# Kernel optimization log

Hardware: AMD Instinct MI355X
Metric: run time of the kernel (lower is better)

The kernel has to match this reference:

```python
import jax, jax.numpy as jnp
import numpy as np

BS, S, H, T = 16, 256, 1024, 32  # batch, num entities, hidden, num relation tags
N_TAGS = 7


def setup_inputs() -> dict:
    key = jax.random.key(0)
    k0, k1, k2, k3 = jax.random.split(key, 4)
    seq_embedding = jax.random.normal(k0, (BS, H), dtype=jnp.float32)
    entities_embeddings = jax.random.normal(k1, (BS, S, H), dtype=jnp.float32)
    entities_tags = jax.random.randint(k2, (BS, S), 0, N_TAGS)
    # relation_classifier: Linear(3*H -> T)
    W = jax.random.normal(k3, (T, 3 * H), dtype=jnp.float32) * 0.02
    b = jnp.zeros((T,), dtype=jnp.float32)
    return {
        "seq_embedding": seq_embedding,
        "entities_embeddings": entities_embeddings,
        "W": W,
        "b": b,
        "entities_tags": entities_tags,
    }


def reference(seq_embedding, entities_embeddings, W, b, entities_tags):
    # Original (eval mode, dropout=identity):
    #   pred[b,i,j] = W @ concat(E[b,i], E[b,j], S[b]) + bias
    # (arg1/arg2/all_seq linears and tag embeddings are dead code in the
    #  original forward: their outputs are never used.)
    # Decompose W = [W1 | W2 | W3] along the feature axis; mathematically
    # identical to materializing the (bs,S,S,3H) concat tensor.
    h = entities_embeddings.shape[-1]
    W1, W2, W3 = W[:, :h], W[:, h:2 * h], W[:, 2 * h:]
    p1 = jnp.einsum('bih,th->bit', entities_embeddings, W1)  # arg1 contribution
    p2 = jnp.einsum('bjh,th->bjt', entities_embeddings, W2)  # arg2 contribution
    ps = seq_embedding @ W3.T + b                             # seq + bias
    # (bs, S, S, T)
    return p1[:, :, None, :] + p2[:, None, :, :] + ps[:, None, None, :]
```

## Files before the change

kernel.cpp:

```cpp
#include <hip/hip_runtime.h>

#define BS 16
#define S  256
#define H  1024
#define T  32

#define PS_OFF 0
#define P1_OFF 512
#define P2_OFF (P1_OFF + BS * S * T)

typedef __bf16 bf16x8 __attribute__((ext_vector_type(8)));
typedef float  f32x4  __attribute__((ext_vector_type(4)));

__global__ __launch_bounds__(256) void gemm_ps(
    const float* __restrict__ seq, const float* __restrict__ E,
    const float* __restrict__ W, const float* __restrict__ bias,
    float* __restrict__ ws)
{
    const int tid = threadIdx.x;
    const int lane = tid & 63, wv = tid >> 6;

    if (blockIdx.x >= 256) {
        float* ps = ws + PS_OFF;
        const int o = (blockIdx.x - 256) * 4 + wv;
        const int bb = o >> 5, t = o & 31;
        const float4* sp = (const float4*)(seq + (size_t)bb * H) + lane * 4;
        const float4* wp = (const float4*)(W + (size_t)t * (3 * H) + 2 * H) + lane * 4;
        float acc = 0.f;
        #pragma unroll
        for (int k = 0; k < 4; ++k) {
            float4 a = sp[k], w = wp[k];
            acc += a.x * w.x + a.y * w.y + a.z * w.z + a.w * w.w;
        }
        #pragma unroll
        for (int m = 32; m >= 1; m >>= 1) acc += __shfl_xor(acc, m);
        if (lane == 0) ps[o] = acc + bias[t];
        return;
    }

    const int m0 = blockIdx.x * 16;
    const int nb = wv * 16;
    const int wrow = nb + (lane & 15);
    const int ksub = (lane >> 4) * 8;

    const float* wbase = W + (size_t)(wrow & 31) * (3 * H) + ((wrow >> 5) ? H : 0) + ksub;
    const float* ebase = E + (size_t)(m0 + (lane & 15)) * H + ksub;

    f32x4 acc[4] = {{0.f,0.f,0.f,0.f},{0.f,0.f,0.f,0.f},
                    {0.f,0.f,0.f,0.f},{0.f,0.f,0.f,0.f}};

    #pragma unroll 8
    for (int s = 0; s < 32; ++s) {
        float4 al = *(const float4*)(ebase + s * 32);
        float4 ah = *(const float4*)(ebase + s * 32 + 4);
        float4 bl = *(const float4*)(wbase + s * 32);
        float4 bh = *(const float4*)(wbase + s * 32 + 4);
        bf16x8 a, b;
        a[0] = (__bf16)al.x; a[1] = (__bf16)al.y; a[2] = (__bf16)al.z; a[3] = (__bf16)al.w;
        a[4] = (__bf16)ah.x; a[5] = (__bf16)ah.y; a[6] = (__bf16)ah.z; a[7] = (__bf16)ah.w;
        b[0] = (__bf16)bl.x; b[1] = (__bf16)bl.y; b[2] = (__bf16)bl.z; b[3] = (__bf16)bl.w;
        b[4] = (__bf16)bh.x; b[5] = (__bf16)bh.y; b[6] = (__bf16)bh.z; b[7] = (__bf16)bh.w;
        acc[s & 3] = __builtin_amdgcn_mfma_f32_16x16x32_bf16(a, b, acc[s & 3], 0, 0, 0);
    }
    f32x4 sum = (acc[0] + acc[1]) + (acc[2] + acc[3]);

    const int orow = (lane >> 4) * 4;
    float* dst = (nb < 32) ? (ws + P1_OFF) : (ws + P2_OFF);
    const int c = wrow & 31;
    #pragma unroll
    for (int r = 0; r < 4; ++r)
        dst[(size_t)(m0 + orow + r) * T + c] = sum[r];
}

__global__ __launch_bounds__(256) void bcast_add(
    const float* __restrict__ ws, float* __restrict__ out)
{
    const int blk = blockIdx.x;
    const int b = blk >> 8, i = blk & 255;
    const int tid = threadIdx.x;

    __shared__ __align__(16) float s1[32];
    if (tid < 32)
        s1[tid] = (ws + P1_OFF)[(size_t)(b * S + i) * T + tid]
                + (ws + PS_OFF)[b * T + tid];
    __syncthreads();

    const float4 s = *(const float4*)&s1[(tid & 7) * 4];
    const float4* p2v = (const float4*)(ws + P2_OFF) + (size_t)b * (S * T / 4);
    float4* ov = (float4*)out + (size_t)(b * S + i) * (S * T / 4);

    #pragma unroll
    for (int k = tid; k < S * T / 4; k += 256) {
        float4 v = p2v[k];
        float4 r;
        r.x = v.x + s.x; r.y = v.y + s.y; r.z = v.z + s.z; r.w = v.w + s.w;
        ov[k] = r;
    }
}

extern "C" void kernel_launch(void* const* d_in, const int* in_sizes, int n_in,
                              void* d_out, int out_size, void* d_ws, size_t ws_size,
                              hipStream_t stream)
{
    const float* seq  = (const float*)d_in[0];
    const float* E    = (const float*)d_in[1];
    const float* W    = (const float*)d_in[2];
    const float* bias = (const float*)d_in[3];
    float* out = (float*)d_out;
    float* ws  = (float*)d_ws;

    gemm_ps<<<384, 256, 0, stream>>>(seq, E, W, bias, ws);
    bcast_add<<<BS * S, 256, 0, stream>>>(ws, out);
}
```

Measured before the change: 45.25 us.

## Stage E tile in LDS for GEMM and emit four rows per broadcast block

The GEMM blocks now load their 16-row E tile cooperatively into shared memory in two K-halves, and prefetch the W fragments into registers, instead of each wave reading E directly from global memory. The seq-projection blocks move to the front of the grid. The broadcast-add kernel now handles four i-rows per block, so each P2 vector read is reused for four output rows and the grid shrinks by four. The broadcast-add stage writes the large output tensor and is bandwidth-bound, so the effect depends mostly on that store path. The GEMM change adds barriers and LDS use.

```diff
diff --git a/kernel.cpp b/kernel.cpp
--- a/kernel.cpp
+++ b/kernel.cpp
@@ -12,6 +12,13 @@
 typedef __bf16 bf16x8 __attribute__((ext_vector_type(8)));
 typedef float  f32x4  __attribute__((ext_vector_type(4)));
 
+__device__ inline bf16x8 to_bf8(float4 lo, float4 hi) {
+    bf16x8 r;
+    r[0] = (__bf16)lo.x; r[1] = (__bf16)lo.y; r[2] = (__bf16)lo.z; r[3] = (__bf16)lo.w;
+    r[4] = (__bf16)hi.x; r[5] = (__bf16)hi.y; r[6] = (__bf16)hi.z; r[7] = (__bf16)hi.w;
+    return r;
+}
+
 __global__ __launch_bounds__(256) void gemm_ps(
     const float* __restrict__ seq, const float* __restrict__ E,
     const float* __restrict__ W, const float* __restrict__ bias,
@@ -20,9 +27,9 @@
     const int tid = threadIdx.x;
     const int lane = tid & 63, wv = tid >> 6;
 
-    if (blockIdx.x >= 256) {
+    if (blockIdx.x < 128) {
         float* ps = ws + PS_OFF;
-        const int o = (blockIdx.x - 256) * 4 + wv;
+        const int o = blockIdx.x * 4 + wv;
         const int bb = o >> 5, t = o & 31;
         const float4* sp = (const float4*)(seq + (size_t)bb * H) + lane * 4;
         const float4* wp = (const float4*)(W + (size_t)t * (3 * H) + 2 * H) + lane * 4;
@@ -38,30 +45,70 @@
         return;
     }
 
-    const int m0 = blockIdx.x * 16;
+    __shared__ __align__(16) float Ef[16][516];
+
+    const int m0 = (blockIdx.x - 128) * 16;
     const int nb = wv * 16;
     const int wrow = nb + (lane & 15);
     const int ksub = (lane >> 4) * 8;
+    const int erow = lane & 15;
 
-    const float* wbase = W + (size_t)(wrow & 31) * (3 * H) + ((wrow >> 5) ? H : 0) + ksub;
-    const float* ebase = E + (size_t)(m0 + (lane & 15)) * H + ksub;
+    const float* wbase = W + (size_t)(wrow & 31) * (3 * H)
+                           + ((wrow >> 5) ? H : 0) + ksub;
 
     f32x4 acc[4] = {{0.f,0.f,0.f,0.f},{0.f,0.f,0.f,0.f},
                     {0.f,0.f,0.f,0.f},{0.f,0.f,0.f,0.f}};
 
-    #pragma unroll 8
-    for (int s = 0; s < 32; ++s) {
-        float4 al = *(const float4*)(ebase + s * 32);
-        float4 ah = *(const float4*)(ebase + s * 32 + 4);
-        float4 bl = *(const float4*)(wbase + s * 32);
-        float4 bh = *(const float4*)(wbase + s * 32 + 4);
-        bf16x8 a, b;
-        a[0] = (__bf16)al.x; a[1] = (__bf16)al.y; a[2] = (__bf16)al.z; a[3] = (__bf16)al.w;
-        a[4] = (__bf16)ah.x; a[5] = (__bf16)ah.y; a[6] = (__bf16)ah.z; a[7] = (__bf16)ah.w;
-        b[0] = (__bf16)bl.x; b[1] = (__bf16)bl.y; b[2] = (__bf16)bl.z; b[3] = (__bf16)bl.w;
-        b[4] = (__bf16)bh.x; b[5] = (__bf16)bh.y; b[6] = (__bf16)bh.z; b[7] = (__bf16)bh.w;
-        acc[s & 3] = __builtin_amdgcn_mfma_f32_16x16x32_bf16(a, b, acc[s & 3], 0, 0, 0);
+    float4 tmp[8];
+    #pragma unroll
+    for (int i = 0; i < 8; ++i) {
+        int f = tid + i * 256, row = f >> 7, c4 = f & 127;
+        tmp[i] = *(const float4*)(E + (size_t)(m0 + row) * H + c4 * 4);
     }
+    #pragma unroll
+    for (int i = 0; i < 8; ++i) {
+        int f = tid + i * 256, row = f >> 7, c4 = f & 127;
+        *(float4*)&Ef[row][c4 * 4] = tmp[i];
+    }
+    bf16x8 bf[16];
+    #pragma unroll
+    for (int s = 0; s < 16; ++s)
+        bf[s] = to_bf8(*(const float4*)(wbase + s * 32),
+                       *(const float4*)(wbase + s * 32 + 4));
+    __syncthreads();
+
+    #pragma unroll
+    for (int s = 0; s < 16; ++s) {
+        const float* e = &Ef[erow][s * 32 + ksub];
+        bf16x8 a = to_bf8(*(const float4*)e, *(const float4*)(e + 4));
+        acc[s & 3] = __builtin_amdgcn_mfma_f32_16x16x32_bf16(a, bf[s], acc[s & 3], 0, 0, 0);
+    }
+
+    #pragma unroll
+    for (int i = 0; i < 8; ++i) {
+        int f = tid + i * 256, row = f >> 7, c4 = f & 127;
+        tmp[i] = *(const float4*)(E + (size_t)(m0 + row) * H + 512 + c4 * 4);
+    }
+    #pragma unroll
+    for (int s = 0; s < 16; ++s)
+        bf[s] = to_bf8(*(const float4*)(wbase + 512 + s * 32),
+                       *(const float4*)(wbase + 512 + s * 32 + 4));
+
+    __syncthreads();
+    #pragma unroll
+    for (int i = 0; i < 8; ++i) {
+        int f = tid + i * 256, row = f >> 7, c4 = f & 127;
+        *(float4*)&Ef[row][c4 * 4] = tmp[i];
+    }
+    __syncthreads();
+
+    #pragma unroll
+    for (int s = 0; s < 16; ++s) {
+        const float* e = &Ef[erow][s * 32 + ksub];
+        bf16x8 a = to_bf8(*(const float4*)e, *(const float4*)(e + 4));
+        acc[s & 3] = __builtin_amdgcn_mfma_f32_16x16x32_bf16(a, bf[s], acc[s & 3], 0, 0, 0);
+    }
+
     f32x4 sum = (acc[0] + acc[1]) + (acc[2] + acc[3]);
 
     const int orow = (lane >> 4) * 4;
@@ -76,25 +123,40 @@
     const float* __restrict__ ws, float* __restrict__ out)
 {
     const int blk = blockIdx.x;
-    const int b = blk >> 8, i = blk & 255;
+    const int b  = blk >> 6;
+    const int i0 = (blk & 63) * 4;
     const int tid = threadIdx.x;
 
-    __shared__ __align__(16) float s1[32];
-    if (tid < 32)
-        s1[tid] = (ws + P1_OFF)[(size_t)(b * S + i) * T + tid]
-                + (ws + PS_OFF)[b * T + tid];
+    __shared__ __align__(16) float s1[4][32];
+    if (tid < 128) {
+        int r = tid >> 5, t = tid & 31;
+        s1[r][t] = (ws + P1_OFF)[(size_t)(b * S + i0 + r) * T + t]
+                 + (ws + PS_OFF)[b * T + t];
+    }
     __syncthreads();
 
-    const float4 s = *(const float4*)&s1[(tid & 7) * 4];
+    const int t4 = (tid & 7) * 4;
+    const float4 s0 = *(const float4*)&s1[0][t4];
+    const float4 s1v = *(const float4*)&s1[1][t4];
+    const float4 s2 = *(const float4*)&s1[2][t4];
+    const float4 s3 = *(const float4*)&s1[3][t4];
+
     const float4* p2v = (const float4*)(ws + P2_OFF) + (size_t)b * (S * T / 4);
-    float4* ov = (float4*)out + (size_t)(b * S + i) * (S * T / 4);
+    float4* o0 = (float4*)out + (size_t)(b * S + i0) * (S * T / 4);
+    const int RS = S * T / 4;
 
     #pragma unroll
-    for (int k = tid; k < S * T / 4; k += 256) {
+    for (int k = tid; k < RS; k += 256) {
         float4 v = p2v[k];
-        float4 r;
-        r.x = v.x + s.x; r.y = v.y + s.y; r.z = v.z + s.z; r.w = v.w + s.w;
-        ov[k] = r;
+        float4 r0, r1, r2, r3;
+        r0.x = v.x + s0.x;  r0.y = v.y + s0.y;  r0.z = v.z + s0.z;  r0.w = v.w + s0.w;
+        r1.x = v.x + s1v.x; r1.y = v.y + s1v.y; r1.z = v.z + s1v.z; r1.w = v.w + s1v.w;
+        r2.x = v.x + s2.x;  r2.y = v.y + s2.y;  r2.z = v.z + s2.z;  r2.w = v.w + s2.w;
+        r3.x = v.x + s3.x;  r3.y = v.y + s3.y;  r3.z = v.z + s3.z;  r3.w = v.w + s3.w;
+        o0[k]          = r0;
+        o0[k + RS]     = r1;
+        o0[k + 2 * RS] = r2;
+        o0[k + 3 * RS] = r3;
     }
 }
 
@@ -110,5 +172,5 @@
     float* ws  = (float*)d_ws;
 
     gemm_ps<<<384, 256, 0, stream>>>(seq, E, W, bias, ws);
-    bcast_add<<<BS * S, 256, 0, stream>>>(ws, out);
+    bcast_add<<<1024, 256, 0, stream>>>(ws, out);
 }
```

After: 53.26 us. 1.18x slower.

## Stage E tile in LDS as bf16 and split K across waves

Applied to the files above, without the earlier changes.

The GEMM part of gemm_ps now loads each 16-row E tile once into shared memory as bf16, instead of having each of the four waves read the same E rows from global memory. Each wave handles a quarter of K for all 64 output columns, holding its W fragments in registers. Partial sums are then reduced across waves through shared memory. The ps blocks are moved to the front of the grid. This cuts redundant global E traffic and conversion work, at the cost of extra LDS use, two barriers and higher register pressure from 32 bf16x8 fragments per lane.

```diff
diff --git a/kernel.cpp b/kernel.cpp
--- a/kernel.cpp
+++ b/kernel.cpp
@@ -12,6 +12,13 @@
 typedef __bf16 bf16x8 __attribute__((ext_vector_type(8)));
 typedef float  f32x4  __attribute__((ext_vector_type(4)));
 
+__device__ inline bf16x8 to_bf8(float4 lo, float4 hi) {
+    bf16x8 r;
+    r[0] = (__bf16)lo.x; r[1] = (__bf16)lo.y; r[2] = (__bf16)lo.z; r[3] = (__bf16)lo.w;
+    r[4] = (__bf16)hi.x; r[5] = (__bf16)hi.y; r[6] = (__bf16)hi.z; r[7] = (__bf16)hi.w;
+    return r;
+}
+
 __global__ __launch_bounds__(256) void gemm_ps(
     const float* __restrict__ seq, const float* __restrict__ E,
     const float* __restrict__ W, const float* __restrict__ bias,
@@ -20,9 +27,9 @@
     const int tid = threadIdx.x;
     const int lane = tid & 63, wv = tid >> 6;
 
-    if (blockIdx.x >= 256) {
+    if (blockIdx.x < 128) {
         float* ps = ws + PS_OFF;
-        const int o = (blockIdx.x - 256) * 4 + wv;
+        const int o = blockIdx.x * 4 + wv;
         const int bb = o >> 5, t = o & 31;
         const float4* sp = (const float4*)(seq + (size_t)bb * H) + lane * 4;
         const float4* wp = (const float4*)(W + (size_t)t * (3 * H) + 2 * H) + lane * 4;
@@ -38,38 +45,66 @@
         return;
     }
 
-    const int m0 = blockIdx.x * 16;
-    const int nb = wv * 16;
-    const int wrow = nb + (lane & 15);
+    __shared__ __align__(16) __bf16 Ebf[16][1032];
+    __shared__ __align__(16) float  pacc[4][16][64];
+
+    const int m0 = (blockIdx.x - 128) * 16;
+
+    #pragma unroll
+    for (int i = 0; i < 8; ++i) {
+        int f = tid + i * 256;
+        int row = f >> 7, c8 = f & 127;
+        const float4* src = (const float4*)(E + (size_t)(m0 + row) * H + c8 * 8);
+        *(bf16x8*)&Ebf[row][c8 * 8] = to_bf8(src[0], src[1]);
+    }
+
+    const int kc = wv * 256;
     const int ksub = (lane >> 4) * 8;
+    bf16x8 bf[32];
+    #pragma unroll
+    for (int nt = 0; nt < 4; ++nt) {
+        const int col = nt * 16 + (lane & 15);
+        const float* wb = W + (size_t)(col & 31) * (3 * H)
+                            + ((col >= 32) ? H : 0) + kc + ksub;
+        #pragma unroll
+        for (int s = 0; s < 8; ++s)
+            bf[nt * 8 + s] = to_bf8(*(const float4*)(wb + s * 32),
+                                    *(const float4*)(wb + s * 32 + 4));
+    }
 
-    const float* wbase = W + (size_t)(wrow & 31) * (3 * H) + ((wrow >> 5) ? H : 0) + ksub;
-    const float* ebase = E + (size_t)(m0 + (lane & 15)) * H + ksub;
+    __syncthreads();
 
     f32x4 acc[4] = {{0.f,0.f,0.f,0.f},{0.f,0.f,0.f,0.f},
                     {0.f,0.f,0.f,0.f},{0.f,0.f,0.f,0.f}};
+    const int erow = lane & 15;
+    #pragma unroll
+    for (int s = 0; s < 8; ++s) {
+        bf16x8 a = *(const bf16x8*)&Ebf[erow][kc + s * 32 + ksub];
+        acc[0] = __builtin_amdgcn_mfma_f32_16x16x32_bf16(a, bf[s],      acc[0], 0, 0, 0);
+        acc[1] = __builtin_amdgcn_mfma_f32_16x16x32_bf16(a, bf[8 + s],  acc[1], 0, 0, 0);
+        acc[2] = __builtin_amdgcn_mfma_f32_16x16x32_bf16(a, bf[16 + s], acc[2], 0, 0, 0);
+        acc[3] = __builtin_amdgcn_mfma_f32_16x16x32_bf16(a, bf[24 + s], acc[3], 0, 0, 0);
+    }
 
-    #pragma unroll 8
-    for (int s = 0; s < 32; ++s) {
-        float4 al = *(const float4*)(ebase + s * 32);
-        float4 ah = *(const float4*)(ebase + s * 32 + 4);
-        float4 bl = *(const float4*)(wbase + s * 32);
-        float4 bh = *(const float4*)(wbase + s * 32 + 4);
-        bf16x8 a, b;
-        a[0] = (__bf16)al.x; a[1] = (__bf16)al.y; a[2] = (__bf16)al.z; a[3] = (__bf16)al.w;
-        a[4] = (__bf16)ah.x; a[5] = (__bf16)ah.y; a[6] = (__bf16)ah.z; a[7] = (__bf16)ah.w;
-        b[0] = (__bf16)bl.x; b[1] = (__bf16)bl.y; b[2] = (__bf16)bl.z; b[3] = (__bf16)bl.w;
-        b[4] = (__bf16)bh.x; b[5] = (__bf16)bh.y; b[6] = (__bf16)bh.z; b[7] = (__bf16)bh.w;
-        acc[s & 3] = __builtin_amdgcn_mfma_f32_16x16x32_bf16(a, b, acc[s & 3], 0, 0, 0);
+    const int prow = (lane >> 4) * 4;
+    #pragma unroll
+    for (int nt = 0; nt < 4; ++nt)
+        #pragma unroll
+        for (int r = 0; r < 4; ++r)
+            pacc[wv][prow + r][nt * 16 + (lane & 15)] = acc[nt][r];
+
+    __syncthreads();
+
+    const int col = tid & 63;
+    const int r0 = tid >> 6;
+    #pragma unroll
+    for (int rr = 0; rr < 4; ++rr) {
+        const int row = r0 + rr * 4;
+        float v = (pacc[0][row][col] + pacc[1][row][col])
+                + (pacc[2][row][col] + pacc[3][row][col]);
+        if (col < 32) (ws + P1_OFF)[(size_t)(m0 + row) * T + col] = v;
+        else          (ws + P2_OFF)[(size_t)(m0 + row) * T + (col - 32)] = v;
     }
-    f32x4 sum = (acc[0] + acc[1]) + (acc[2] + acc[3]);
-
-    const int orow = (lane >> 4) * 4;
-    float* dst = (nb < 32) ? (ws + P1_OFF) : (ws + P2_OFF);
-    const int c = wrow & 31;
-    #pragma unroll
-    for (int r = 0; r < 4; ++r)
-        dst[(size_t)(m0 + orow + r) * T + c] = sum[r];
 }
 
 __global__ __launch_bounds__(256) void bcast_add(
```

New measurement: 43.66 us. 3.5% less time.
